# Optimization experiments

Measured on AMD Instinct MI355X. Metric: run time of the kernel, lower is better.

## Reference

```python
import jax, jax.numpy as jnp
import numpy as np

B, N, E, D_IN, D_ENC, D_GNN, D_FC, N_CLS = 16, 5000, 160000, 128, 256, 256, 128, 2


def setup_inputs() -> dict:
    key = jax.random.key(0)
    ks = jax.random.split(key, 16)
    sc = lambda d: 1.0 / np.sqrt(d)
    x = jax.random.normal(ks[0], (B, N, D_IN), dtype=jnp.float32)
    edge_index = jax.random.randint(ks[1], (B, 2, E), 0, N, dtype=jnp.int64)
    return {
        "x": x,
        "edge_index": edge_index,
        "We": jax.random.normal(ks[2], (D_IN, D_ENC), jnp.float32) * sc(D_IN),
        "be": jnp.zeros((D_ENC,), jnp.float32),
        "Wl1": jax.random.normal(ks[3], (D_ENC, D_ENC), jnp.float32) * sc(D_ENC),
        "bl1": jnp.zeros((D_ENC,), jnp.float32),
        "Wr1": jax.random.normal(ks[4], (D_ENC, D_ENC), jnp.float32) * sc(D_ENC),
        "Wl2": jax.random.normal(ks[5], (D_ENC, D_GNN), jnp.float32) * sc(D_ENC),
        "bl2": jnp.zeros((D_GNN,), jnp.float32),
        "Wr2": jax.random.normal(ks[6], (D_ENC, D_GNN), jnp.float32) * sc(D_ENC),
        "Wlp": jax.random.normal(ks[7], (D_ENC, 1), jnp.float32) * sc(D_ENC),
        "blp": jnp.zeros((1,), jnp.float32),
        "Wrp": jax.random.normal(ks[8], (D_ENC, 1), jnp.float32) * sc(D_ENC),
        "Wc1": jax.random.normal(ks[9], (D_GNN, D_FC), jnp.float32) * sc(D_GNN),
        "bc1": jnp.zeros((D_FC,), jnp.float32),
        "Wc2": jax.random.normal(ks[10], (D_FC, N_CLS), jnp.float32) * sc(D_FC),
        "bc2": jnp.zeros((N_CLS,), jnp.float32),
    }


def _sage(x, src, dst, Wl, bl, Wr):
    # PyG SAGEConv (mean aggr): lin_l(mean_{j in N(i)} x_j) + lin_r(x_i)
    agg = jax.ops.segment_sum(x[src], dst, num_segments=N)            # [N, d]
    deg = jax.ops.segment_sum(jnp.ones((src.shape[0], 1), x.dtype), dst, num_segments=N)
    mean = agg / jnp.maximum(deg, 1.0)
    return mean @ Wl + bl + x @ Wr


def reference(x, edge_index, We, be, Wl1, bl1, Wr1, Wl2, bl2, Wr2,
              Wlp, blp, Wrp, Wc1, bc1, Wc2, bc2):
    def one_bag(xb, eib):
        src, dst = eib[0], eib[1]
        h = jax.nn.relu(xb @ We + be)                                  # encoder -> [N, d_enc]
        # GNNConvStack (raw_last=False: activation after every layer)
        g = jax.nn.relu(_sage(h, src, dst, Wl1, bl1, Wr1))
        g = jax.nn.relu(_sage(g, src, dst, Wl2, bl2, Wr2))             # [N, d_gnn]
        # pooling SAGEConv on encoder output, softmax over nodes (dim=0)
        cw = jax.nn.softmax(_sage(h, src, dst, Wlp, blp, Wrp), axis=0) # [N, 1]
        # dense_diff_pool re-softmaxes s over clusters (dim=-1); with 1 cluster -> ones
        s = jax.nn.softmax(cw, axis=-1)                                # [N, 1]
        emb = (s.T @ g)[0]                                             # [d_gnn]
        # classifier (raw_last=True)
        h1 = jax.nn.relu(emb @ Wc1 + bc1)
        return h1 @ Wc2 + bc2                                          # [n_classes]

    return jax.vmap(one_bag)(x, edge_index)                           # [B, n_classes]
```

## Files before the change

kernel.cpp:

```cpp
#include <hip/hip_runtime.h>
#include <hip/hip_bf16.h>
#include <cstdint>
#include <cstddef>

#define NBAGS  16
#define NNODES 5000
#define NEDGES 160000
#define DIN    128
#define DENC   256
#define DFC    128
#define NCLS   2

#define TPB 40
#define HB  32
#define HEPB (NEDGES / HB)

typedef __attribute__((ext_vector_type(8))) short short8;
typedef __attribute__((ext_vector_type(4))) float f32x4;
typedef unsigned int uint32x4 __attribute__((ext_vector_type(4)));

static __device__ __forceinline__ ushort f2b(float v) {
    __hip_bfloat16 b = __float2bfloat16(v);
    return *reinterpret_cast<ushort*>(&b);
}

template<bool DUAL, bool RELU, bool REDUCE>
__device__ __forceinline__
void gemm_body(int bx, char* smem,
               const ushort* __restrict__ A1, const ushort* __restrict__ Wt1,
               const ushort* __restrict__ A2, const ushort* __restrict__ Wt2,
               const float* __restrict__ bias, ushort* __restrict__ C,
               float* __restrict__ emb, int K)
{
    ushort* As = (ushort*)smem;
    ushort* Bs = As + 4096;

    const int bag  = bx & 15;
    const int rem  = bx >> 4;
    const int col  = rem & 1;
    const int tile = rem >> 1;
    const size_t bagRow0 = (size_t)bag * NNODES;
    const int rloc0 = tile * 128;
    const int n0 = col * 128;

    const int tid  = threadIdx.x;
    const int wave = tid >> 6;
    const int lane = tid & 63;
    const int quad = lane >> 4;
    const int l16  = lane & 15;
    const int wm   = (wave >> 1) * 64;
    const int wn   = (wave & 1) * 64;

    f32x4 acc[4][4];
#pragma unroll
    for (int i = 0; i < 4; ++i)
#pragma unroll
        for (int j = 0; j < 4; ++j)
#pragma unroll
            for (int r = 0; r < 4; ++r) acc[i][j][r] = 0.f;

    const int sr = tid >> 1;
    const int sc = (tid & 1) * 2;
    const int sk = sc * 8;

    const int npass = DUAL ? 2 : 1;
    for (int pass = 0; pass < npass; ++pass) {
        const ushort* __restrict__ A = (DUAL && pass) ? A2 : A1;
        const ushort* __restrict__ W = (DUAL && pass) ? Wt2 : Wt1;

        for (int k0 = 0; k0 < K; k0 += 32) {
            {
                uint4 v0 = make_uint4(0, 0, 0, 0), v1 = make_uint4(0, 0, 0, 0);
                const int rl = rloc0 + sr;
                if (rl < NNODES) {
                    const uint4* src = (const uint4*)(A + (bagRow0 + rl) * K + k0 + sk);
                    v0 = src[0]; v1 = src[1];
                }
                *(uint4*)&As[(sc * 128 + sr) * 8]       = v0;
                *(uint4*)&As[((sc + 1) * 128 + sr) * 8] = v1;
            }
            {
                const uint4* src = (const uint4*)(W + (size_t)(n0 + sr) * K + k0 + sk);
                *(uint4*)&Bs[(sc * 128 + sr) * 8]       = src[0];
                *(uint4*)&Bs[((sc + 1) * 128 + sr) * 8] = src[1];
            }
            __syncthreads();

            short8 af[4], bf[4];
#pragma unroll
            for (int t = 0; t < 4; ++t) {
                af[t] = *(const short8*)&As[(quad * 128 + wm + t * 16 + l16) * 8];
                bf[t] = *(const short8*)&Bs[(quad * 128 + wn + t * 16 + l16) * 8];
            }
#pragma unroll
            for (int tm = 0; tm < 4; ++tm)
#pragma unroll
                for (int tn = 0; tn < 4; ++tn)
                    acc[tm][tn] = __builtin_amdgcn_mfma_f32_16x16x32_bf16(
                        af[tm], bf[tn], acc[tm][tn], 0, 0, 0);
            __syncthreads();
        }
    }

    if (!REDUCE) {
#pragma unroll
        for (int tm = 0; tm < 4; ++tm) {
            const int rbase = rloc0 + wm + tm * 16 + quad * 4;
#pragma unroll
            for (int reg = 0; reg < 4; ++reg) {
                const int rl = rbase + reg;
                if (rl < NNODES) {
#pragma unroll
                    for (int tn = 0; tn < 4; ++tn) {
                        const int gcol = n0 + wn + tn * 16 + l16;
                        float v = acc[tm][tn][reg] + bias[gcol];
                        if (RELU) v = fmaxf(v, 0.f);
                        C[(bagRow0 + rl) * 256 + gcol] = f2b(v);
                    }
                }
            }
        }
    } else {
        float* red = (float*)smem;
        if (tid < 128) red[tid] = 0.f;
        __syncthreads();
#pragma unroll
        for (int tn = 0; tn < 4; ++tn) {
            const int cl = wn + tn * 16 + l16;
            const float bv = bias[n0 + cl];
            float p = 0.f;
#pragma unroll
            for (int tm = 0; tm < 4; ++tm) {
#pragma unroll
                for (int reg = 0; reg < 4; ++reg) {
                    const int rl = rloc0 + wm + tm * 16 + quad * 4 + reg;
                    float v = acc[tm][tn][reg] + bv;
                    if (RELU) v = fmaxf(v, 0.f);
                    if (rl < NNODES) p += v;
                }
            }
            atomicAdd(&red[cl], p);
        }
        __syncthreads();
        if (tid < 128)
            atomicAdd(&emb[bag * DENC + n0 + tid], red[tid]);
    }
}

template<bool DUAL, bool RELU, bool REDUCE>
__global__ __launch_bounds__(256)
void gemm_bf16_kernel(const ushort* __restrict__ A1, const ushort* __restrict__ Wt1,
                      const ushort* __restrict__ A2, const ushort* __restrict__ Wt2,
                      const float* __restrict__ bias, ushort* __restrict__ C,
                      float* __restrict__ emb, int K)
{
    __shared__ __align__(16) char smem[16384];
    gemm_body<DUAL, RELU, REDUCE>(blockIdx.x, smem, A1, Wt1, A2, Wt2, bias, C, emb, K);
}

__device__ __forceinline__
void place_body(int pbx, char* smem, const int* __restrict__ edges,
                const int* __restrict__ histG, const int* __restrict__ rowptr,
                ushort* __restrict__ colidx)
{
    const int bag = pbx & 15;
    const int blk = pbx >> 4;
    int* h = (int*)smem;
    const int* __restrict__ rel = histG + ((size_t)bag * HB + blk) * NNODES;
    const int* __restrict__ rp  = rowptr + bag * (NNODES + 1);
    for (int i = threadIdx.x; i < NNODES; i += 256) h[i] = rp[i] + rel[i];
    __syncthreads();
    const int* __restrict__ eb = edges + (size_t)bag * 2 * NEDGES;
    ushort* __restrict__ co = colidx + (size_t)bag * NEDGES;
    const int e0 = blk * HEPB;
    for (int r = threadIdx.x; r < HEPB; r += 256) {
        const int s = __builtin_nontemporal_load(&eb[e0 + r]);
        const int d = __builtin_nontemporal_load(&eb[NEDGES + e0 + r]);
        const int pos = atomicAdd(&h[d], 1);
        co[pos] = (ushort)s;
    }
}

__global__ __launch_bounds__(256)
void enc_place_kernel(const ushort* __restrict__ xb, const ushort* __restrict__ Wet,
                      const float* __restrict__ be, ushort* __restrict__ H,
                      const int* __restrict__ edges, const int* __restrict__ histG,
                      const int* __restrict__ rowptr, ushort* __restrict__ colidx)
{
    __shared__ __align__(16) char smem[20480];
    if (blockIdx.x < NBAGS * TPB * 2)
        gemm_body<false, true, false>(blockIdx.x, smem, xb, Wet, nullptr, nullptr,
                                      be, H, nullptr, DIN);
    else
        place_body(blockIdx.x - NBAGS * TPB * 2, smem, edges, histG, rowptr, colidx);
}

#define HIST_B (NBAGS * HB)
#define CVT_B  (NBAGS * 625)
#define WTE_B  128
#define WTW_B  1024
#define PREP_GRID (HIST_B + CVT_B + WTE_B + WTW_B)

__global__ __launch_bounds__(256)
void prep_kernel(const int* __restrict__ edges, int* __restrict__ histG,
                 const float* __restrict__ x, ushort* __restrict__ xb,
                 const float* __restrict__ We,  ushort* __restrict__ Wet,
                 const float* __restrict__ Wl1, ushort* __restrict__ Wl1t,
                 const float* __restrict__ Wr1, ushort* __restrict__ Wr1t,
                 const float* __restrict__ Wl2, ushort* __restrict__ Wl2t,
                 const float* __restrict__ Wr2, ushort* __restrict__ Wr2t)
{
    __shared__ int sh[NNODES];
    const int bx = blockIdx.x;
    if (bx < HIST_B) {
        const int bag = bx & 15;
        const int blk = bx >> 4;
        for (int i = threadIdx.x; i < NNODES; i += 256) sh[i] = 0;
        __syncthreads();
        const int* __restrict__ dstp =
            edges + (size_t)bag * 2 * NEDGES + NEDGES + blk * HEPB;
        for (int r = threadIdx.x; r < HEPB; r += 256)
            atomicAdd(&sh[__builtin_nontemporal_load(&dstp[r])], 1);
        __syncthreads();
        int* __restrict__ out = histG + ((size_t)bag * HB + blk) * NNODES;
        for (int i = threadIdx.x; i < NNODES; i += 256) out[i] = sh[i];
    } else if (bx < HIST_B + CVT_B) {
        const int cbx = bx - HIST_B;
        const int bag = cbx & 15;
        const int chunk = cbx >> 4;
        const size_t base = (size_t)bag * (NNODES * DIN / 4);
        const int i = chunk * 256 + threadIdx.x;
        const float4 v = ((const float4*)x)[base + i];
        ushort4 o;
        o.x = f2b(v.x); o.y = f2b(v.y); o.z = f2b(v.z); o.w = f2b(v.w);
        ((ushort4*)xb)[base + i] = o;
    } else if (bx < HIST_B + CVT_B + WTE_B) {
        const int idx = (bx - HIST_B - CVT_B) * 256 + threadIdx.x;
        const int n = idx / DIN;
        const int k = idx - n * DIN;
        Wet[idx] = f2b(We[k * 256 + n]);
    } else {
        const int r = bx - HIST_B - CVT_B - WTE_B;
        const int which = r >> 8;
        const int idx = (r & 255) * 256 + threadIdx.x;
        const int n = idx >> 8;
        const int k = idx & 255;
        const float* W  = (which == 0) ? Wl1 : (which == 1) ? Wr1 : (which == 2) ? Wl2 : Wr2;
        ushort* Wt      = (which == 0) ? Wl1t : (which == 1) ? Wr1t : (which == 2) ? Wl2t : Wr2t;
        Wt[idx] = f2b(W[k * 256 + n]);
    }
}

__global__ __launch_bounds__(256)
void colsum_kernel(int* __restrict__ histG, int* __restrict__ cnt)
{
    const int bag = blockIdx.x & 15;
    const int chunk = blockIdx.x >> 4;
    const int node = chunk * 256 + threadIdx.x;
    if (node >= NNODES) return;
    int* __restrict__ hb = histG + (size_t)bag * HB * NNODES + node;
    int run = 0;
#pragma unroll 8
    for (int blk = 0; blk < HB; ++blk) {
        int* p = hb + blk * NNODES;
        const int v = *p;
        *p = run;
        run += v;
    }
    cnt[bag * NNODES + node] = run;
}

__global__ __launch_bounds__(1024)
void scan_kernel(const int* __restrict__ cnt, int* __restrict__ rowptr)
{
    const int b = blockIdx.x;
    const int t = threadIdx.x;
    __shared__ int sh[1024];
    const int CH = 5;
    const int base = t * CH;
    int local[CH];
    int sum = 0;
#pragma unroll
    for (int i = 0; i < CH; ++i) {
        const int g = base + i;
        const int v = (g < NNODES) ? cnt[b * NNODES + g] : 0;
        local[i] = v; sum += v;
    }
    sh[t] = sum;
    __syncthreads();
    for (int off = 1; off < 1024; off <<= 1) {
        const int add = (t >= off) ? sh[t - off] : 0;
        __syncthreads();
        sh[t] += add;
        __syncthreads();
    }
    int run = sh[t] - sum;
#pragma unroll
    for (int i = 0; i < CH; ++i) {
        const int g = base + i;
        if (g < NNODES) rowptr[b * (NNODES + 1) + g] = run;
        run += local[i];
    }
    if (t == 1023) rowptr[b * (NNODES + 1) + NNODES] = run;
}

__global__ __launch_bounds__(256)
void agg_mean_kernel(const ushort* __restrict__ X, const int* __restrict__ rowptr,
                     const ushort* __restrict__ colidx, ushort* __restrict__ M,
                     int batchBase)
{
    const int bx = blockIdx.x;
    const int bag = batchBase + (bx & 7);
    const int grp = bx >> 3;
    const int wave = threadIdx.x >> 6;
    const int lane = threadIdx.x & 63;
    const int half = lane >> 5;
    const int hl = lane & 31;
    const int node = grp * 4 + wave;

    const int* rp = rowptr + bag * (NNODES + 1);
    const int s = rp[node];
    const int e = rp[node + 1];
    const float inv = 1.0f / fmaxf((float)(e - s), 1.0f);
    const uint32x4* __restrict__ Xb = (const uint32x4*)(X + (size_t)bag * NNODES * DENC);
    const ushort* __restrict__ ci = colidx + (size_t)bag * NEDGES;

    float2 a0 = {0.f, 0.f}, a1 = {0.f, 0.f}, a2 = {0.f, 0.f}, a3 = {0.f, 0.f};

    int j = s;
    for (; j + 8 <= e; j += 8) {
        int idx[4];
#pragma unroll
        for (int t = 0; t < 4; ++t) idx[t] = ci[j + 2 * t + half];
        uint32x4 u[4];
#pragma unroll
        for (int t = 0; t < 4; ++t) u[t] = Xb[idx[t] * 32 + hl];
#pragma unroll
        for (int t = 0; t < 4; ++t) {
            a0.x += __uint_as_float(u[t].x << 16);
            a0.y += __uint_as_float(u[t].x & 0xffff0000u);
            a1.x += __uint_as_float(u[t].y << 16);
            a1.y += __uint_as_float(u[t].y & 0xffff0000u);
            a2.x += __uint_as_float(u[t].z << 16);
            a2.y += __uint_as_float(u[t].z & 0xffff0000u);
            a3.x += __uint_as_float(u[t].w << 16);
            a3.y += __uint_as_float(u[t].w & 0xffff0000u);
        }
    }
    for (; j < e; j += 2) {
        const int jj = j + half;
        uint32x4 u = {0u, 0u, 0u, 0u};
        if (jj < e) u = Xb[(int)ci[jj] * 32 + hl];
        a0.x += __uint_as_float(u.x << 16);
        a0.y += __uint_as_float(u.x & 0xffff0000u);
        a1.x += __uint_as_float(u.y << 16);
        a1.y += __uint_as_float(u.y & 0xffff0000u);
        a2.x += __uint_as_float(u.z << 16);
        a2.y += __uint_as_float(u.z & 0xffff0000u);
        a3.x += __uint_as_float(u.w << 16);
        a3.y += __uint_as_float(u.w & 0xffff0000u);
    }

    a0.x += __shfl_xor(a0.x, 32); a0.y += __shfl_xor(a0.y, 32);
    a1.x += __shfl_xor(a1.x, 32); a1.y += __shfl_xor(a1.y, 32);
    a2.x += __shfl_xor(a2.x, 32); a2.y += __shfl_xor(a2.y, 32);
    a3.x += __shfl_xor(a3.x, 32); a3.y += __shfl_xor(a3.y, 32);

    if (half == 0) {
        uint32x4 o;
        o.x = (uint32_t)f2b(a0.x * inv) | ((uint32_t)f2b(a0.y * inv) << 16);
        o.y = (uint32_t)f2b(a1.x * inv) | ((uint32_t)f2b(a1.y * inv) << 16);
        o.z = (uint32_t)f2b(a2.x * inv) | ((uint32_t)f2b(a2.y * inv) << 16);
        o.w = (uint32_t)f2b(a3.x * inv) | ((uint32_t)f2b(a3.y * inv) << 16);
        uint32x4* dst = (uint32x4*)(M + ((size_t)bag * NNODES + node) * DENC) + hl;
        __builtin_nontemporal_store(o, dst);
    }
}

__global__ __launch_bounds__(128)
void classifier_kernel(const float* __restrict__ emb, const float* __restrict__ Wc1,
                       const float* __restrict__ bc1, const float* __restrict__ Wc2,
                       const float* __restrict__ bc2, float* __restrict__ out)
{
    const int b = blockIdx.x;
    const int t = threadIdx.x;
    __shared__ float se[DENC];
    se[t] = emb[b * DENC + t];
    se[128 + t] = emb[b * DENC + 128 + t];
    __syncthreads();
    float h = bc1[t];
    for (int k = 0; k < DENC; ++k) h = fmaf(se[k], Wc1[k * DFC + t], h);
    h = fmaxf(h, 0.f);
    __shared__ float s0[128], s1[128];
    s0[t] = h * Wc2[t * NCLS + 0];
    s1[t] = h * Wc2[t * NCLS + 1];
    __syncthreads();
    for (int off = 64; off > 0; off >>= 1) {
        if (t < off) { s0[t] += s0[t + off]; s1[t] += s1[t + off]; }
        __syncthreads();
    }
    if (t == 0) {
        out[b * NCLS + 0] = s0[0] + bc2[0];
        out[b * NCLS + 1] = s1[0] + bc2[1];
    }
}

extern "C" void kernel_launch(void* const* d_in, const int* in_sizes, int n_in,
                              void* d_out, int out_size, void* d_ws, size_t ws_size,
                              hipStream_t stream)
{
    const float* x    = (const float*)d_in[0];
    const int*   edges= (const int*)d_in[1];
    const float* We   = (const float*)d_in[2];
    const float* be   = (const float*)d_in[3];
    const float* Wl1  = (const float*)d_in[4];
    const float* bl1  = (const float*)d_in[5];
    const float* Wr1  = (const float*)d_in[6];
    const float* Wl2  = (const float*)d_in[7];
    const float* bl2  = (const float*)d_in[8];
    const float* Wr2  = (const float*)d_in[9];
    const float* Wc1  = (const float*)d_in[13];
    const float* bc1  = (const float*)d_in[14];
    const float* Wc2  = (const float*)d_in[15];
    const float* bc2  = (const float*)d_in[16];
    float* out = (float*)d_out;

    auto rnd = [](size_t v) { return (v + 255) & ~(size_t)255; };
    char* p = (char*)d_ws;
    auto alloc = [&](size_t bytes) -> char* {
        char* r = p; p += rnd(bytes); return r;
    };
    ushort* xb    = (ushort*)alloc((size_t)NBAGS * NNODES * DIN * 2);
    ushort* H     = (ushort*)alloc((size_t)NBAGS * NNODES * DENC * 2);
    ushort* Mb    = (ushort*)alloc((size_t)NBAGS * NNODES * DENC * 2);
    ushort* Gb    = (ushort*)alloc((size_t)NBAGS * NNODES * DENC * 2);
    ushort* Wet   = (ushort*)alloc((size_t)256 * DIN * 2);
    ushort* Wl1t  = (ushort*)alloc((size_t)256 * DENC * 2);
    ushort* Wr1t  = (ushort*)alloc((size_t)256 * DENC * 2);
    ushort* Wl2t  = (ushort*)alloc((size_t)256 * DENC * 2);
    ushort* Wr2t  = (ushort*)alloc((size_t)256 * DENC * 2);
    int*    rowptr= (int*)   alloc((size_t)NBAGS * (NNODES + 1) * 4);
    int*    cnt   = (int*)   alloc((size_t)NBAGS * NNODES * 4);
    int*    histG = (int*)   alloc((size_t)NBAGS * HB * NNODES * 4);
    ushort* colidx= (ushort*)alloc((size_t)NBAGS * NEDGES * 2);
    float*  emb   = (float*) alloc((size_t)NBAGS * DENC * 4);

    (void)hipMemsetAsync(emb, 0, (size_t)NBAGS * DENC * 4, stream);

    prep_kernel<<<PREP_GRID, 256, 0, stream>>>(
        edges, histG, x, xb, We, Wet, Wl1, Wl1t, Wr1, Wr1t, Wl2, Wl2t, Wr2, Wr2t);

    colsum_kernel<<<NBAGS * 20, 256, 0, stream>>>(histG, cnt);
    scan_kernel<<<NBAGS, 1024, 0, stream>>>(cnt, rowptr);

    enc_place_kernel<<<NBAGS * TPB * 2 + HIST_B, 256, 0, stream>>>(
        xb, Wet, be, H, edges, histG, rowptr, colidx);

    const int gemm_grid = NBAGS * TPB * 2;
    const int agg_grid  = 8 * (NNODES / 4);

    agg_mean_kernel<<<agg_grid, 256, 0, stream>>>(H, rowptr, colidx, Mb, 0);
    agg_mean_kernel<<<agg_grid, 256, 0, stream>>>(H, rowptr, colidx, Mb, 8);
    gemm_bf16_kernel<true, true, false><<<gemm_grid, 256, 0, stream>>>(
        Mb, Wl1t, H, Wr1t, bl1, Gb, nullptr, DENC);

    agg_mean_kernel<<<agg_grid, 256, 0, stream>>>(Gb, rowptr, colidx, H, 0);
    agg_mean_kernel<<<agg_grid, 256, 0, stream>>>(Gb, rowptr, colidx, H, 8);
    gemm_bf16_kernel<true, true, true><<<gemm_grid, 256, 0, stream>>>(
        H, Wl2t, Gb, Wr2t, bl2, nullptr, emb, DENC);

    classifier_kernel<<<NBAGS, 128, 0, stream>>>(emb, Wc1, bc1, Wc2, bc2, out);
}
```

Before: 412.0 us.

## Double-buffer shared-memory tiles in bf16 GEMM with register prefetch

Restructures the GEMM main loop to use two LDS buffers: the next K-tile is loaded from global memory into registers while MFMAs run on the current tile, then stored into the alternate buffer. This removes one barrier per iteration and hides global load latency behind compute. The cost is twice the shared memory per block (32 KB), which may reduce occupancy, plus higher register pressure from the prefetch registers. An extra barrier is added before the reduction epilogue reuses shared memory.

Result: no change. 414.9 us (+0.7%).

```diff
diff --git a/kernel.cpp b/kernel.cpp
--- a/kernel.cpp
+++ b/kernel.cpp
@@ -32,8 +32,8 @@
                const float* __restrict__ bias, ushort* __restrict__ C,
                float* __restrict__ emb, int K)
 {
-    ushort* As = (ushort*)smem;
-    ushort* Bs = As + 4096;
+    ushort* As0 = (ushort*)smem;
+    ushort* Bs0 = As0 + 2 * 4096;
 
     const int bag  = bx & 15;
     const int rem  = bx >> 4;
@@ -63,41 +63,61 @@
     const int sc = (tid & 1) * 2;
     const int sk = sc * 8;
 
-    const int npass = DUAL ? 2 : 1;
-    for (int pass = 0; pass < npass; ++pass) {
-        const ushort* __restrict__ A = (DUAL && pass) ? A2 : A1;
-        const ushort* __restrict__ W = (DUAL && pass) ? Wt2 : Wt1;
-
-        for (int k0 = 0; k0 < K; k0 += 32) {
-            {
-                uint4 v0 = make_uint4(0, 0, 0, 0), v1 = make_uint4(0, 0, 0, 0);
-                const int rl = rloc0 + sr;
-                if (rl < NNODES) {
-                    const uint4* src = (const uint4*)(A + (bagRow0 + rl) * K + k0 + sk);
-                    v0 = src[0]; v1 = src[1];
-                }
-                *(uint4*)&As[(sc * 128 + sr) * 8]       = v0;
-                *(uint4*)&As[((sc + 1) * 128 + sr) * 8] = v1;
-            }
-            {
-                const uint4* src = (const uint4*)(W + (size_t)(n0 + sr) * K + k0 + sk);
-                *(uint4*)&Bs[(sc * 128 + sr) * 8]       = src[0];
-                *(uint4*)&Bs[((sc + 1) * 128 + sr) * 8] = src[1];
-            }
-            __syncthreads();
-
-            short8 af[4], bf[4];
-#pragma unroll
-            for (int t = 0; t < 4; ++t) {
-                af[t] = *(const short8*)&As[(quad * 128 + wm + t * 16 + l16) * 8];
-                bf[t] = *(const short8*)&Bs[(quad * 128 + wn + t * 16 + l16) * 8];
-            }
-#pragma unroll
-            for (int tm = 0; tm < 4; ++tm)
-#pragma unroll
-                for (int tn = 0; tn < 4; ++tn)
-                    acc[tm][tn] = __builtin_amdgcn_mfma_f32_16x16x32_bf16(
-                        af[tm], bf[tn], acc[tm][tn], 0, 0, 0);
+    const int IPP = K / 32;
+    const int NIT = (DUAL ? 2 : 1) * IPP;
+
+    uint4 ra0, ra1, rb0, rb1;
+
+    auto issue_load = [&](int it) {
+        const int pass = DUAL ? ((it >= IPP) ? 1 : 0) : 0;
+        const ushort* __restrict__ A = pass ? A2 : A1;
+        const ushort* __restrict__ W = pass ? Wt2 : Wt1;
+        const int k0 = (it - pass * IPP) * 32;
+        ra0 = make_uint4(0, 0, 0, 0); ra1 = make_uint4(0, 0, 0, 0);
+        const int rl = rloc0 + sr;
+        if (rl < NNODES) {
+            const uint4* src = (const uint4*)(A + (bagRow0 + rl) * K + k0 + sk);
+            ra0 = src[0]; ra1 = src[1];
+        }
+        const uint4* wsrc = (const uint4*)(W + (size_t)(n0 + sr) * K + k0 + sk);
+        rb0 = wsrc[0]; rb1 = wsrc[1];
+    };
+    auto store_tile = [&](int buf) {
+        ushort* As = As0 + buf * 4096;
+        ushort* Bs = Bs0 + buf * 4096;
+        *(uint4*)&As[(sc * 128 + sr) * 8]       = ra0;
+        *(uint4*)&As[((sc + 1) * 128 + sr) * 8] = ra1;
+        *(uint4*)&Bs[(sc * 128 + sr) * 8]       = rb0;
+        *(uint4*)&Bs[((sc + 1) * 128 + sr) * 8] = rb1;
+    };
+
+    issue_load(0);
+    store_tile(0);
+    __syncthreads();
+
+#pragma unroll 2
+    for (int it = 0; it < NIT; ++it) {
+        const int cur = it & 1;
+        const bool more = (it + 1 < NIT);
+        if (more) issue_load(it + 1);
+
+        const ushort* As = As0 + cur * 4096;
+        const ushort* Bs = Bs0 + cur * 4096;
+        short8 af[4], bf[4];
+#pragma unroll
+        for (int t = 0; t < 4; ++t) {
+            af[t] = *(const short8*)&As[(quad * 128 + wm + t * 16 + l16) * 8];
+            bf[t] = *(const short8*)&Bs[(quad * 128 + wn + t * 16 + l16) * 8];
+        }
+#pragma unroll
+        for (int tm = 0; tm < 4; ++tm)
+#pragma unroll
+            for (int tn = 0; tn < 4; ++tn)
+                acc[tm][tn] = __builtin_amdgcn_mfma_f32_16x16x32_bf16(
+                    af[tm], bf[tn], acc[tm][tn], 0, 0, 0);
+
+        if (more) {
+            store_tile((it + 1) & 1);
             __syncthreads();
         }
     }
@@ -121,6 +141,7 @@
             }
         }
     } else {
+        __syncthreads();
         float* red = (float*)smem;
         if (tid < 128) red[tid] = 0.f;
         __syncthreads();
@@ -154,7 +175,7 @@
                       const float* __restrict__ bias, ushort* __restrict__ C,
                       float* __restrict__ emb, int K)
 {
-    __shared__ __align__(16) char smem[16384];
+    __shared__ __align__(16) char smem[32768];
     gemm_body<DUAL, RELU, REDUCE>(blockIdx.x, smem, A1, Wt1, A2, Wt2, bias, C, emb, K);
 }
 
@@ -187,7 +208,7 @@
                       const int* __restrict__ edges, const int* __restrict__ histG,
                       const int* __restrict__ rowptr, ushort* __restrict__ colidx)
 {
-    __shared__ __align__(16) char smem[20480];
+    __shared__ __align__(16) char smem[32768];
     if (blockIdx.x < NBAGS * TPB * 2)
         gemm_body<false, true, false>(blockIdx.x, smem, xb, Wet, nullptr, nullptr,
                                       be, H, nullptr, DIN);
```

## Overlap half-batch GEMM with next half's aggregation in fused kernels; use 512-thread blocks

Applied to the files above, without the earlier changes.

Splits the per-layer work into two 8-bag halves and fuses each half's dual GEMM with the other half's neighbour-mean aggregation in a single launch. GEMM blocks and gather blocks then run concurrently, so compute-bound MFMA work can hide memory-bound gathers. All kernels also move to 512 threads per block: the GEMM wave tile shrinks to 32x64, and aggregation processes 8 nodes per block. The cost is more careful buffer ordering across launches, since Mb, H and Gb are reused between halves, and a smaller per-wave GEMM tile that gets less register reuse.

Result: slower. 485.3 us (+17.8%).

```diff
diff --git a/kernel.cpp b/kernel.cpp
--- a/kernel.cpp
+++ b/kernel.cpp
@@ -11,9 +11,14 @@
 #define DFC    128
 #define NCLS   2
 
-#define TPB 40
 #define HB  32
 #define HEPB (NEDGES / HB)
+#define GT  512
+
+#define ENC_GEMM_B (16 * 40 * 2)
+#define GEMM_H_B   (8 * 40 * 2)
+#define AGG_B      (8 * 625)
+#define FUSED_GRID (GEMM_H_B + AGG_B)
 
 typedef __attribute__((ext_vector_type(8))) short short8;
 typedef __attribute__((ext_vector_type(4))) float f32x4;
@@ -26,7 +31,7 @@
 
 template<bool DUAL, bool RELU, bool REDUCE>
 __device__ __forceinline__
-void gemm_body(int bx, char* smem,
+void gemm_body(int bag, int tile, int col, char* smem,
                const ushort* __restrict__ A1, const ushort* __restrict__ Wt1,
                const ushort* __restrict__ A2, const ushort* __restrict__ Wt2,
                const float* __restrict__ bias, ushort* __restrict__ C,
@@ -35,10 +40,6 @@
     ushort* As = (ushort*)smem;
     ushort* Bs = As + 4096;
 
-    const int bag  = bx & 15;
-    const int rem  = bx >> 4;
-    const int col  = rem & 1;
-    const int tile = rem >> 1;
     const size_t bagRow0 = (size_t)bag * NNODES;
     const int rloc0 = tile * 128;
     const int n0 = col * 128;
@@ -48,20 +49,20 @@
     const int lane = tid & 63;
     const int quad = lane >> 4;
     const int l16  = lane & 15;
-    const int wm   = (wave >> 1) * 64;
+    const int wm   = (wave >> 1) * 32;
     const int wn   = (wave & 1) * 64;
 
-    f32x4 acc[4][4];
-#pragma unroll
-    for (int i = 0; i < 4; ++i)
+    f32x4 acc[2][4];
+#pragma unroll
+    for (int i = 0; i < 2; ++i)
 #pragma unroll
         for (int j = 0; j < 4; ++j)
 #pragma unroll
             for (int r = 0; r < 4; ++r) acc[i][j][r] = 0.f;
 
-    const int sr = tid >> 1;
-    const int sc = (tid & 1) * 2;
-    const int sk = sc * 8;
+    const int srow = tid & 127;
+    const int schk = tid >> 7;
+    const int sk = schk * 8;
 
     const int npass = DUAL ? 2 : 1;
     for (int pass = 0; pass < npass; ++pass) {
@@ -69,31 +70,25 @@
         const ushort* __restrict__ W = (DUAL && pass) ? Wt2 : Wt1;
 
         for (int k0 = 0; k0 < K; k0 += 32) {
-            {
-                uint4 v0 = make_uint4(0, 0, 0, 0), v1 = make_uint4(0, 0, 0, 0);
-                const int rl = rloc0 + sr;
-                if (rl < NNODES) {
-                    const uint4* src = (const uint4*)(A + (bagRow0 + rl) * K + k0 + sk);
-                    v0 = src[0]; v1 = src[1];
-                }
-                *(uint4*)&As[(sc * 128 + sr) * 8]       = v0;
-                *(uint4*)&As[((sc + 1) * 128 + sr) * 8] = v1;
-            }
-            {
-                const uint4* src = (const uint4*)(W + (size_t)(n0 + sr) * K + k0 + sk);
-                *(uint4*)&Bs[(sc * 128 + sr) * 8]       = src[0];
-                *(uint4*)&Bs[((sc + 1) * 128 + sr) * 8] = src[1];
-            }
+            uint4 va = make_uint4(0, 0, 0, 0);
+            const int rl = rloc0 + srow;
+            if (rl < NNODES)
+                va = *(const uint4*)(A + (bagRow0 + rl) * K + k0 + sk);
+            const uint4 vb = *(const uint4*)(W + (size_t)(n0 + srow) * K + k0 + sk);
+
+            *(uint4*)&As[(schk * 128 + srow) * 8] = va;
+            *(uint4*)&Bs[(schk * 128 + srow) * 8] = vb;
             __syncthreads();
 
-            short8 af[4], bf[4];
-#pragma unroll
-            for (int t = 0; t < 4; ++t) {
+            short8 af[2], bf[4];
+#pragma unroll
+            for (int t = 0; t < 2; ++t)
                 af[t] = *(const short8*)&As[(quad * 128 + wm + t * 16 + l16) * 8];
+#pragma unroll
+            for (int t = 0; t < 4; ++t)
                 bf[t] = *(const short8*)&Bs[(quad * 128 + wn + t * 16 + l16) * 8];
-            }
-#pragma unroll
-            for (int tm = 0; tm < 4; ++tm)
+#pragma unroll
+            for (int tm = 0; tm < 2; ++tm)
 #pragma unroll
                 for (int tn = 0; tn < 4; ++tn)
                     acc[tm][tn] = __builtin_amdgcn_mfma_f32_16x16x32_bf16(
@@ -104,7 +99,7 @@
 
     if (!REDUCE) {
 #pragma unroll
-        for (int tm = 0; tm < 4; ++tm) {
+        for (int tm = 0; tm < 2; ++tm) {
             const int rbase = rloc0 + wm + tm * 16 + quad * 4;
 #pragma unroll
             for (int reg = 0; reg < 4; ++reg) {
@@ -130,7 +125,7 @@
             const float bv = bias[n0 + cl];
             float p = 0.f;
 #pragma unroll
-            for (int tm = 0; tm < 4; ++tm) {
+            for (int tm = 0; tm < 2; ++tm) {
 #pragma unroll
                 for (int reg = 0; reg < 4; ++reg) {
                     const int rl = rloc0 + wm + tm * 16 + quad * 4 + reg;
@@ -147,15 +142,120 @@
     }
 }
 
-template<bool DUAL, bool RELU, bool REDUCE>
-__global__ __launch_bounds__(256)
-void gemm_bf16_kernel(const ushort* __restrict__ A1, const ushort* __restrict__ Wt1,
+__device__ __forceinline__
+void agg_body(int local, int base, const ushort* __restrict__ X,
+              const int* __restrict__ rowptr, const ushort* __restrict__ colidx,
+              ushort* __restrict__ M)
+{
+    const int bag = base + (local & 7);
+    const int grp = local >> 3;
+    const int wave = threadIdx.x >> 6;
+    const int lane = threadIdx.x & 63;
+    const int half = lane >> 5;
+    const int hl = lane & 31;
+    const int node = grp * 8 + wave;
+
+    const int* rp = rowptr + bag * (NNODES + 1);
+    const int s = rp[node];
+    const int e = rp[node + 1];
+    const float inv = 1.0f / fmaxf((float)(e - s), 1.0f);
+    const uint32x4* __restrict__ Xb = (const uint32x4*)(X + (size_t)bag * NNODES * DENC);
+    const ushort* __restrict__ ci = colidx + (size_t)bag * NEDGES;
+
+    float2 a0 = {0.f, 0.f}, a1 = {0.f, 0.f}, a2 = {0.f, 0.f}, a3 = {0.f, 0.f};
+
+    int j = s;
+    for (; j + 8 <= e; j += 8) {
+        int idx[4];
+#pragma unroll
+        for (int t = 0; t < 4; ++t) idx[t] = ci[j + 2 * t + half];
+        uint32x4 u[4];
+#pragma unroll
+        for (int t = 0; t < 4; ++t) u[t] = Xb[idx[t] * 32 + hl];
+#pragma unroll
+        for (int t = 0; t < 4; ++t) {
+            a0.x += __uint_as_float(u[t].x << 16);
+            a0.y += __uint_as_float(u[t].x & 0xffff0000u);
+            a1.x += __uint_as_float(u[t].y << 16);
+            a1.y += __uint_as_float(u[t].y & 0xffff0000u);
+            a2.x += __uint_as_float(u[t].z << 16);
+            a2.y += __uint_as_float(u[t].z & 0xffff0000u);
+            a3.x += __uint_as_float(u[t].w << 16);
+            a3.y += __uint_as_float(u[t].w & 0xffff0000u);
+        }
+    }
+    for (; j < e; j += 2) {
+        const int jj = j + half;
+        uint32x4 u = {0u, 0u, 0u, 0u};
+        if (jj < e) u = Xb[(int)ci[jj] * 32 + hl];
+        a0.x += __uint_as_float(u.x << 16);
+        a0.y += __uint_as_float(u.x & 0xffff0000u);
+        a1.x += __uint_as_float(u.y << 16);
+        a1.y += __uint_as_float(u.y & 0xffff0000u);
+        a2.x += __uint_as_float(u.z << 16);
+        a2.y += __uint_as_float(u.z & 0xffff0000u);
+        a3.x += __uint_as_float(u.w << 16);
+        a3.y += __uint_as_float(u.w & 0xffff0000u);
+    }
+
+    a0.x += __shfl_xor(a0.x, 32); a0.y += __shfl_xor(a0.y, 32);
+    a1.x += __shfl_xor(a1.x, 32); a1.y += __shfl_xor(a1.y, 32);
+    a2.x += __shfl_xor(a2.x, 32); a2.y += __shfl_xor(a2.y, 32);
+    a3.x += __shfl_xor(a3.x, 32); a3.y += __shfl_xor(a3.y, 32);
+
+    if (half == 0) {
+        uint32x4 o;
+        o.x = (uint32_t)f2b(a0.x * inv) | ((uint32_t)f2b(a0.y * inv) << 16);
+        o.y = (uint32_t)f2b(a1.x * inv) | ((uint32_t)f2b(a1.y * inv) << 16);
+        o.z = (uint32_t)f2b(a2.x * inv) | ((uint32_t)f2b(a2.y * inv) << 16);
+        o.w = (uint32_t)f2b(a3.x * inv) | ((uint32_t)f2b(a3.y * inv) << 16);
+        uint32x4* dst = (uint32x4*)(M + ((size_t)bag * NNODES + node) * DENC) + hl;
+        __builtin_nontemporal_store(o, dst);
+    }
+}
+
+template<bool REDUCE>
+__global__ __launch_bounds__(GT)
+void fused_layer_kernel(const ushort* __restrict__ A1, const ushort* __restrict__ Wt1,
+                        const ushort* __restrict__ A2, const ushort* __restrict__ Wt2,
+                        const float* __restrict__ bias, ushort* __restrict__ C,
+                        float* __restrict__ emb, int gemmBase,
+                        const ushort* __restrict__ aggX, const int* __restrict__ rowptr,
+                        const ushort* __restrict__ colidx, ushort* __restrict__ aggM,
+                        int aggBase)
+{
+    __shared__ __align__(16) char smem[16384];
+    const int bx = blockIdx.x;
+    if (bx < GEMM_H_B) {
+        const int bag = gemmBase + (bx & 7);
+        const int rem = bx >> 3;
+        gemm_body<true, true, REDUCE>(bag, rem >> 1, rem & 1, smem,
+                                      A1, Wt1, A2, Wt2, bias, C, emb, DENC);
+    } else {
+        agg_body(bx - GEMM_H_B, aggBase, aggX, rowptr, colidx, aggM);
+    }
+}
+
+template<bool REDUCE>
+__global__ __launch_bounds__(GT)
+void gemm_half_kernel(const ushort* __restrict__ A1, const ushort* __restrict__ Wt1,
                       const ushort* __restrict__ A2, const ushort* __restrict__ Wt2,
                       const float* __restrict__ bias, ushort* __restrict__ C,
-                      float* __restrict__ emb, int K)
+                      float* __restrict__ emb, int gemmBase)
 {
     __shared__ __align__(16) char smem[16384];
-    gemm_body<DUAL, RELU, REDUCE>(blockIdx.x, smem, A1, Wt1, A2, Wt2, bias, C, emb, K);
+    const int bag = gemmBase + (blockIdx.x & 7);
+    const int rem = blockIdx.x >> 3;
+    gemm_body<true, true, REDUCE>(bag, rem >> 1, rem & 1, smem,
+                                  A1, Wt1, A2, Wt2, bias, C, emb, DENC);
+}
+
+__global__ __launch_bounds__(GT)
+void agg_mean_kernel(const ushort* __restrict__ X, const int* __restrict__ rowptr,
+                     const ushort* __restrict__ colidx, ushort* __restrict__ M,
+                     int base)
+{
+    agg_body(blockIdx.x, base, X, rowptr, colidx, M);
 }
 
 __device__ __forceinline__
@@ -168,12 +268,12 @@
     int* h = (int*)smem;
     const int* __restrict__ rel = histG + ((size_t)bag * HB + blk) * NNODES;
     const int* __restrict__ rp  = rowptr + bag * (NNODES + 1);
-    for (int i = threadIdx.x; i < NNODES; i += 256) h[i] = rp[i] + rel[i];
+    for (int i = threadIdx.x; i < NNODES; i += GT) h[i] = rp[i] + rel[i];
     __syncthreads();
     const int* __restrict__ eb = edges + (size_t)bag * 2 * NEDGES;
     ushort* __restrict__ co = colidx + (size_t)bag * NEDGES;
     const int e0 = blk * HEPB;
-    for (int r = threadIdx.x; r < HEPB; r += 256) {
+    for (int r = threadIdx.x; r < HEPB; r += GT) {
         const int s = __builtin_nontemporal_load(&eb[e0 + r]);
         const int d = __builtin_nontemporal_load(&eb[NEDGES + e0 + r]);
         const int pos = atomicAdd(&h[d], 1);
@@ -181,18 +281,22 @@
     }
 }
 
-__global__ __launch_bounds__(256)
+__global__ __launch_bounds__(GT)
 void enc_place_kernel(const ushort* __restrict__ xb, const ushort* __restrict__ Wet,
                       const float* __restrict__ be, ushort* __restrict__ H,
                       const int* __restrict__ edges, const int* __restrict__ histG,
                       const int* __restrict__ rowptr, ushort* __restrict__ colidx)
 {
     __shared__ __align__(16) char smem[20480];
-    if (blockIdx.x < NBAGS * TPB * 2)
-        gemm_body<false, true, false>(blockIdx.x, smem, xb, Wet, nullptr, nullptr,
-                                      be, H, nullptr, DIN);
-    else
-        place_body(blockIdx.x - NBAGS * TPB * 2, smem, edges, histG, rowptr, colidx);
+    const int bx = blockIdx.x;
+    if (bx < ENC_GEMM_B) {
+        const int bag = bx & 15;
+        const int rem = bx >> 4;
+        gemm_body<false, true, false>(bag, rem >> 1, rem & 1, smem,
+                                      xb, Wet, nullptr, nullptr, be, H, nullptr, DIN);
+    } else {
+        place_body(bx - ENC_GEMM_B, smem, edges, histG, rowptr, colidx);
+    }
 }
 
 #define HIST_B (NBAGS * HB)
@@ -304,79 +408,6 @@
     if (t == 1023) rowptr[b * (NNODES + 1) + NNODES] = run;
 }
 
-__global__ __launch_bounds__(256)
-void agg_mean_kernel(const ushort* __restrict__ X, const int* __restrict__ rowptr,
-                     const ushort* __restrict__ colidx, ushort* __restrict__ M,
-                     int batchBase)
-{
-    const int bx = blockIdx.x;
-    const int bag = batchBase + (bx & 7);
-    const int grp = bx >> 3;
-    const int wave = threadIdx.x >> 6;
-    const int lane = threadIdx.x & 63;
-    const int half = lane >> 5;
-    const int hl = lane & 31;
-    const int node = grp * 4 + wave;
-
-    const int* rp = rowptr + bag * (NNODES + 1);
-    const int s = rp[node];
-    const int e = rp[node + 1];
-    const float inv = 1.0f / fmaxf((float)(e - s), 1.0f);
-    const uint32x4* __restrict__ Xb = (const uint32x4*)(X + (size_t)bag * NNODES * DENC);
-    const ushort* __restrict__ ci = colidx + (size_t)bag * NEDGES;
-
-    float2 a0 = {0.f, 0.f}, a1 = {0.f, 0.f}, a2 = {0.f, 0.f}, a3 = {0.f, 0.f};
-
-    int j = s;
-    for (; j + 8 <= e; j += 8) {
-        int idx[4];
-#pragma unroll
-        for (int t = 0; t < 4; ++t) idx[t] = ci[j + 2 * t + half];
-        uint32x4 u[4];
-#pragma unroll
-        for (int t = 0; t < 4; ++t) u[t] = Xb[idx[t] * 32 + hl];
-#pragma unroll
-        for (int t = 0; t < 4; ++t) {
-            a0.x += __uint_as_float(u[t].x << 16);
-            a0.y += __uint_as_float(u[t].x & 0xffff0000u);
-            a1.x += __uint_as_float(u[t].y << 16);
-            a1.y += __uint_as_float(u[t].y & 0xffff0000u);
-            a2.x += __uint_as_float(u[t].z << 16);
-            a2.y += __uint_as_float(u[t].z & 0xffff0000u);
-            a3.x += __uint_as_float(u[t].w << 16);
-            a3.y += __uint_as_float(u[t].w & 0xffff0000u);
-        }
-    }
-    for (; j < e; j += 2) {
-        const int jj = j + half;
-        uint32x4 u = {0u, 0u, 0u, 0u};
-        if (jj < e) u = Xb[(int)ci[jj] * 32 + hl];
-        a0.x += __uint_as_float(u.x << 16);
-        a0.y += __uint_as_float(u.x & 0xffff0000u);
-        a1.x += __uint_as_float(u.y << 16);
-        a1.y += __uint_as_float(u.y & 0xffff0000u);
-        a2.x += __uint_as_float(u.z << 16);
-        a2.y += __uint_as_float(u.z & 0xffff0000u);
-        a3.x += __uint_as_float(u.w << 16);
-        a3.y += __uint_as_float(u.w & 0xffff0000u);
-    }
-
-    a0.x += __shfl_xor(a0.x, 32); a0.y += __shfl_xor(a0.y, 32);
-    a1.x += __shfl_xor(a1.x, 32); a1.y += __shfl_xor(a1.y, 32);
-    a2.x += __shfl_xor(a2.x, 32); a2.y += __shfl_xor(a2.y, 32);
-    a3.x += __shfl_xor(a3.x, 32); a3.y += __shfl_xor(a3.y, 32);
-
-    if (half == 0) {
-        uint32x4 o;
-        o.x = (uint32_t)f2b(a0.x * inv) | ((uint32_t)f2b(a0.y * inv) << 16);
-        o.y = (uint32_t)f2b(a1.x * inv) | ((uint32_t)f2b(a1.y * inv) << 16);
-        o.z = (uint32_t)f2b(a2.x * inv) | ((uint32_t)f2b(a2.y * inv) << 16);
-        o.w = (uint32_t)f2b(a3.x * inv) | ((uint32_t)f2b(a3.y * inv) << 16);
-        uint32x4* dst = (uint32x4*)(M + ((size_t)bag * NNODES + node) * DENC) + hl;
-        __builtin_nontemporal_store(o, dst);
-    }
-}
-
 __global__ __launch_bounds__(128)
 void classifier_kernel(const float* __restrict__ emb, const float* __restrict__ Wc1,
                        const float* __restrict__ bc1, const float* __restrict__ Wc2,
@@ -453,21 +484,21 @@
     colsum_kernel<<<NBAGS * 20, 256, 0, stream>>>(histG, cnt);
     scan_kernel<<<NBAGS, 1024, 0, stream>>>(cnt, rowptr);
 
-    enc_place_kernel<<<NBAGS * TPB * 2 + HIST_B, 256, 0, stream>>>(
+    enc_place_kernel<<<ENC_GEMM_B + HIST_B, GT, 0, stream>>>(
         xb, Wet, be, H, edges, histG, rowptr, colidx);
 
-    const int gemm_grid = NBAGS * TPB * 2;
-    const int agg_grid  = 8 * (NNODES / 4);
-
-    agg_mean_kernel<<<agg_grid, 256, 0, stream>>>(H, rowptr, colidx, Mb, 0);
-    agg_mean_kernel<<<agg_grid, 256, 0, stream>>>(H, rowptr, colidx, Mb, 8);
-    gemm_bf16_kernel<true, true, false><<<gemm_grid, 256, 0, stream>>>(
-        Mb, Wl1t, H, Wr1t, bl1, Gb, nullptr, DENC);
-
-    agg_mean_kernel<<<agg_grid, 256, 0, stream>>>(Gb, rowptr, colidx, H, 0);
-    agg_mean_kernel<<<agg_grid, 256, 0, stream>>>(Gb, rowptr, colidx, H, 8);
-    gemm_bf16_kernel<true, true, true><<<gemm_grid, 256, 0, stream>>>(
-        H, Wl2t, Gb, Wr2t, bl2, nullptr, emb, DENC);
+    agg_mean_kernel<<<AGG_B, GT, 0, stream>>>(H, rowptr, colidx, Mb, 0);
+    fused_layer_kernel<false><<<FUSED_GRID, GT, 0, stream>>>(
+        Mb, Wl1t, H, Wr1t, bl1, Gb, nullptr, 0,
+        H, rowptr, colidx, Mb, 8);
+    fused_layer_kernel<false><<<FUSED_GRID, GT, 0, stream>>>(
+        Mb, Wl1t, H, Wr1t, bl1, Gb, nullptr, 8,
+        Gb, rowptr, colidx, H, 0);
+    fused_layer_kernel<true><<<FUSED_GRID, GT, 0, stream>>>(
+        H, Wl2t, Gb, Wr2t, bl2, nullptr, emb, 0,
+        Gb, rowptr, colidx, H, 8);
+    gemm_half_kernel<true><<<GEMM_H_B, GT, 0, stream>>>(
+        H, Wl2t, Gb, Wr2t, bl2, nullptr, emb, 8);
 
     classifier_kernel<<<NBAGS, 128, 0, stream>>>(emb, Wc1, bc1, Wc2, bc2, out);
 }
```
